# Optimization experiments

Measured on AMD Instinct MI355X. Metric: run time of the kernel, lower is better.

## Reference

```python
import jax, jax.numpy as jnp
import numpy as np

D_MODEL = 1024
NHEAD = 16
HEAD_DIM = D_MODEL // NHEAD


def setup_inputs() -> dict:
    key = jax.random.key(0)
    ks = jax.random.split(key, 7)
    B, S = 4, 2048
    scale = 1.0 / np.sqrt(D_MODEL)
    x = jax.random.normal(ks[0], (B, S, D_MODEL), dtype=jnp.float32)
    Wq = jax.random.normal(ks[1], (D_MODEL, D_MODEL), dtype=jnp.float32) * scale
    Wk = jax.random.normal(ks[2], (D_MODEL, D_MODEL), dtype=jnp.float32) * scale
    Wv = jax.random.normal(ks[3], (D_MODEL, D_MODEL), dtype=jnp.float32) * scale
    bq = jax.random.normal(ks[4], (D_MODEL,), dtype=jnp.float32) * 0.01
    bk = jax.random.normal(ks[5], (D_MODEL,), dtype=jnp.float32) * 0.01
    bv = jax.random.normal(ks[6], (D_MODEL,), dtype=jnp.float32) * 0.01
    return {"x": x, "Wq": Wq, "bq": bq, "Wk": Wk, "bk": bk, "Wv": Wv, "bv": bv}


def reference(x, Wq, bq, Wk, bk, Wv, bv):
    B, S, _ = x.shape
    # Linear projections (torch Linear: x @ W.T + b; weights here are already [in, out])
    q = x @ Wq + bq
    k = x @ Wk + bk
    v = x @ Wv + bv
    # [B, S, H, Dh] -> [B, H, S, Dh]
    q = q.reshape(B, S, NHEAD, HEAD_DIM).transpose(0, 2, 1, 3)
    k = k.reshape(B, S, NHEAD, HEAD_DIM).transpose(0, 2, 1, 3)
    v = v.reshape(B, S, NHEAD, HEAD_DIM).transpose(0, 2, 1, 3)
    # NOTE: original scales by sqrt(d_model), not sqrt(head_dim)
    scores = jnp.einsum("bhqd,bhkd->bhqk", q, k) / np.sqrt(D_MODEL).astype(np.float32)
    attn = jax.nn.softmax(scores, axis=-1)  # dropout is identity at eval
    out = jnp.einsum("bhqk,bhkd->bhqd", attn, v)
    out = out.transpose(0, 2, 1, 3).reshape(B, S, D_MODEL)
    return out
```

## Files before the change

kernel.cpp:

```cpp
#include <hip/hip_runtime.h>
#include <cstdint>
#include <cstddef>

#define SEQ 2048
#define BATCH 4
#define KVB 64
#define NT (SEQ / KVB)

typedef __attribute__((ext_vector_type(8))) unsigned short u16x8;
typedef __attribute__((ext_vector_type(8))) __bf16 bf16x8;
typedef __attribute__((ext_vector_type(4))) float f32x4;
typedef __attribute__((ext_vector_type(4))) unsigned short u16x4;

#if defined(__has_builtin)
#if __has_builtin(__builtin_amdgcn_exp2f)
#define EXP2(x) __builtin_amdgcn_exp2f(x)
#else
#define EXP2(x) exp2f(x)
#endif
#else
#define EXP2(x) exp2f(x)
#endif

static __device__ __forceinline__ unsigned short f2bf(float f) {
  unsigned u = __builtin_bit_cast(unsigned, f);
  u += 0x7fffu + ((u >> 16) & 1u);
  return (unsigned short)(u >> 16);
}

static __device__ __forceinline__ f32x4 mfma16(u16x8 a, u16x8 b, f32x4 c) {
  return __builtin_amdgcn_mfma_f32_16x16x32_bf16(
      __builtin_bit_cast(bf16x8, a), __builtin_bit_cast(bf16x8, b), c, 0, 0, 0);
}

static __device__ __forceinline__ f32x4 mfma16b(u16x8 a, bf16x8 b, f32x4 c) {
  return __builtin_amdgcn_mfma_f32_16x16x32_bf16(
      __builtin_bit_cast(bf16x8, a), b, c, 0, 0, 0);
}

static __device__ __forceinline__ void gl_lds16(const void* g, void* l) {
  __builtin_amdgcn_global_load_lds(
      (const __attribute__((address_space(1))) void*)g,
      (__attribute__((address_space(3))) void*)l, 16, 0, 0);
}

__global__ __launch_bounds__(256) void k_conv_x(const float* __restrict__ x,
                                                unsigned short* __restrict__ xb) {
  int i = (blockIdx.x * 256 + threadIdx.x) * 8;
  f32x4 a = *reinterpret_cast<const f32x4*>(x + i);
  f32x4 b = *reinterpret_cast<const f32x4*>(x + i + 4);
  u16x8 v;
  v[0] = f2bf(a[0]); v[1] = f2bf(a[1]); v[2] = f2bf(a[2]); v[3] = f2bf(a[3]);
  v[4] = f2bf(b[0]); v[5] = f2bf(b[1]); v[6] = f2bf(b[2]); v[7] = f2bf(b[3]);
  *reinterpret_cast<u16x8*>(xb + i) = v;
}

__global__ __launch_bounds__(256) void k_conv_w(const float* __restrict__ Wq,
                                                const float* __restrict__ Wk,
                                                const float* __restrict__ Wv,
                                                unsigned short* __restrict__ wt) {
  const float* W = (blockIdx.z == 0) ? Wq : (blockIdx.z == 1) ? Wk : Wv;
  unsigned short* dst = wt + (size_t)blockIdx.z * 1024 * 1024;
  __shared__ float tile[32][33];
  int n0 = blockIdx.x * 32, k0 = blockIdx.y * 32;
  int tx = threadIdx.x, ty = threadIdx.y;
#pragma unroll
  for (int i = 0; i < 4; i++) {
    int k = ty + i * 8;
    tile[k][tx] = W[(size_t)(k0 + k) * 1024 + n0 + tx];
  }
  __syncthreads();
#pragma unroll
  for (int i = 0; i < 4; i++) {
    int n = ty + i * 8;
    dst[(size_t)(n0 + n) * 1024 + k0 + tx] = f2bf(tile[tx][n]);
  }
}

__global__ __launch_bounds__(256) void k_qkv_gemm(
    const unsigned short* __restrict__ xb, const unsigned short* __restrict__ wt,
    const float* __restrict__ bq, const float* __restrict__ bk,
    const float* __restrict__ bv,
    unsigned short* __restrict__ qb, unsigned short* __restrict__ kb,
    unsigned short* __restrict__ vt) {
  __shared__ unsigned short Ah[128 * 32];
  __shared__ unsigned short Bh[128 * 32];
  const int tid = threadIdx.x;
  const int lane = tid & 63, wid = tid >> 6;
  const int ln = lane & 15, g = lane >> 4;
  const int wr = wid >> 1, wc = wid & 1;
  const int z = blockIdx.z;
  const int m0 = blockIdx.y * 128, n0 = blockIdx.x * 128;
  const unsigned short* Bt = wt + (size_t)z * 1024 * 1024;

  f32x4 acc[4][4];
#pragma unroll
  for (int i = 0; i < 4; i++)
#pragma unroll
    for (int j = 0; j < 4; j++) acc[i][j] = f32x4{0.f, 0.f, 0.f, 0.f};

  const int sA = wid * 64 + lane;
  const int rA0 = sA >> 2, cA0 = sA & 3;
  const int rA1 = rA0 + 64;

  const unsigned short* gA0 = xb + (size_t)(m0 + rA0) * 1024 + cA0 * 8;
  const unsigned short* gA1 = xb + (size_t)(m0 + rA1) * 1024 + cA0 * 8;
  const unsigned short* gB0 = Bt + (size_t)(n0 + rA0) * 1024 + cA0 * 8;
  const unsigned short* gB1 = Bt + (size_t)(n0 + rA1) * 1024 + cA0 * 8;
  unsigned short* lA0 = Ah + wid * 512;
  unsigned short* lA1 = Ah + 2048 + wid * 512;
  unsigned short* lB0 = Bh + wid * 512;
  unsigned short* lB1 = Bh + 2048 + wid * 512;

  for (int k0 = 0; k0 < 1024; k0 += 32) {
    gl_lds16(gA0 + k0, lA0);
    gl_lds16(gA1 + k0, lA1);
    gl_lds16(gB0 + k0, lB0);
    gl_lds16(gB1 + k0, lB1);
    __syncthreads();
    u16x8 af[4], bfv[4];
#pragma unroll
    for (int mi = 0; mi < 4; mi++)
      af[mi] = *reinterpret_cast<const u16x8*>(&Ah[(wr * 64 + mi * 16 + ln) * 32 + g * 8]);
#pragma unroll
    for (int ni = 0; ni < 4; ni++)
      bfv[ni] = *reinterpret_cast<const u16x8*>(&Bh[(wc * 64 + ni * 16 + ln) * 32 + g * 8]);
#pragma unroll
    for (int mi = 0; mi < 4; mi++)
#pragma unroll
      for (int ni = 0; ni < 4; ni++)
        acc[mi][ni] = mfma16(af[mi], bfv[ni], acc[mi][ni]);
    __syncthreads();
  }

  const float* bias = (z == 0) ? bq : (z == 1) ? bk : bv;
#pragma unroll
  for (int ni = 0; ni < 4; ni++) {
    int n = n0 + wc * 64 + ni * 16 + ln;
    float bb = bias[n];
    int h = n >> 6, d = n & 63;
#pragma unroll
    for (int mi = 0; mi < 4; mi++) {
      int mb = m0 + wr * 64 + mi * 16 + 4 * g;
      int b = mb >> 11, s = mb & 2047;
      if (z == 2) {
        u16x4 pv;
#pragma unroll
        for (int i = 0; i < 4; i++) pv[i] = f2bf(acc[mi][ni][i] + bb);
        int s4 = s >> 2;
        int u = s4 & 7, blk = s4 >> 3;
        int nu = ((u & 3) << 1) | (u >> 2);
        int sp = ((blk << 3) | nu) << 2;
        *reinterpret_cast<u16x4*>(
            &vt[((size_t)((b * 16 + h) * 64 + d)) * 2048 + sp]) = pv;
      } else {
        unsigned short* dst = (z == 0) ? qb : kb;
        float sc = (z == 0) ? 0.0450842200f : 1.0f;
#pragma unroll
        for (int i = 0; i < 4; i++) {
          dst[((size_t)((b * 16 + h) * 2048) + (s + i)) * 64 + d] =
              f2bf((acc[mi][ni][i] + bb) * sc);
        }
      }
    }
  }
}

__global__ __launch_bounds__(512) void k_attn(
    const unsigned short* __restrict__ qb, const unsigned short* __restrict__ kb,
    const unsigned short* __restrict__ vt, float* __restrict__ out) {
  __shared__ unsigned short Kl[2][KVB * 64];
  __shared__ unsigned short Vl[2][64 * KVB];
  const int tid = threadIdx.x;
  const int lane = tid & 63, wid = tid >> 6;
  const int ln = lane & 15, g = lane >> 4;
  const int flat = blockIdx.x;
  const int bh = flat & 63, qidx = flat >> 6;
  const int b = bh >> 4, h = bh & 15;
  const int q0 = qidx * 256 + wid * 32;
  const unsigned short* Qp = qb + (size_t)bh * SEQ * 64;
  const unsigned short* Kp = kb + (size_t)bh * SEQ * 64;
  const unsigned short* Vp = vt + (size_t)bh * 64 * SEQ;

  const int kr0 = tid >> 3;
  const int psw = ((tid & 7) ^ (kr0 & 7)) << 3;
  const unsigned short* srcK0 = Kp + (size_t)kr0 * 64 + psw;
  const unsigned short* srcV0 = Vp + (size_t)kr0 * SEQ + psw;

#define STAGE(bb, tt)                                                     \
  do {                                                                    \
    gl_lds16(srcK0 + (size_t)(tt) * (KVB * 64), &Kl[bb][wid * 512]);      \
    gl_lds16(srcV0 + (size_t)(tt) * KVB, &Vl[bb][wid * 512]);             \
  } while (0)

  u16x8 qf[2][2];
#pragma unroll
  for (int qt = 0; qt < 2; qt++)
#pragma unroll
    for (int dc = 0; dc < 2; dc++)
      qf[qt][dc] = *reinterpret_cast<const u16x8*>(
          &Qp[(size_t)(q0 + qt * 16 + ln) * 64 + dc * 32 + g * 8]);

  f32x4 o[4][2];
#pragma unroll
  for (int dt = 0; dt < 4; dt++)
#pragma unroll
    for (int qt = 0; qt < 2; qt++) o[dt][qt] = f32x4{0.f, 0.f, 0.f, 0.f};
  f32x4 lsum[2] = {f32x4{0.f, 0.f, 0.f, 0.f}, f32x4{0.f, 0.f, 0.f, 0.f}};

  u16x8 ones;
#pragma unroll
  for (int i = 0; i < 8; i++) ones[i] = 0x3F80;

  const int lm = ln & 7;
  const int ksw0 = (g ^ lm) << 3;
  const int ksw1 = ((4 + g) ^ lm) << 3;
  const int vsw0 = (g ^ lm) << 3;
  const int vsw1 = ((4 + g) ^ lm) << 3;

  int buf = 0;
  STAGE(0, 0);
  __syncthreads();

  for (int t = 0; t < NT; t++) {
    if (t + 1 < NT) STAGE(buf ^ 1, t + 1);

    const unsigned short* Kb = Kl[buf];
    const unsigned short* Vb = Vl[buf];

    u16x8 kf[4][2];
#pragma unroll
    for (int kt = 0; kt < 4; kt++) {
      int rb = (kt * 16 + ln) * 64;
      kf[kt][0] = *reinterpret_cast<const u16x8*>(&Kb[rb + ksw0]);
      kf[kt][1] = *reinterpret_cast<const u16x8*>(&Kb[rb + ksw1]);
    }

    f32x4 st[2][4];
    __builtin_amdgcn_s_setprio(1);
#pragma unroll
    for (int qt = 0; qt < 2; qt++)
#pragma unroll
      for (int kt = 0; kt < 4; kt++) {
        f32x4 c = f32x4{0.f, 0.f, 0.f, 0.f};
        c = mfma16(kf[kt][0], qf[qt][0], c);
        c = mfma16(kf[kt][1], qf[qt][1], c);
        st[qt][kt] = c;
      }
    __builtin_amdgcn_s_setprio(0);

#pragma unroll
    for (int qt = 0; qt < 2; qt++)
#pragma unroll
      for (int kt = 0; kt < 4; kt++)
#pragma unroll
        for (int i = 0; i < 4; i++)
          st[qt][kt][i] = EXP2(st[qt][kt][i]);

    bf16x8 pb[2][2];
#pragma unroll
    for (int qt = 0; qt < 2; qt++)
#pragma unroll
      for (int ks = 0; ks < 2; ks++)
#pragma unroll
        for (int i = 0; i < 4; i++) {
          pb[qt][ks][i] = (__bf16)st[qt][2 * ks][i];
          pb[qt][ks][4 + i] = (__bf16)st[qt][2 * ks + 1][i];
        }

    __builtin_amdgcn_s_setprio(1);
#pragma unroll
    for (int dt = 0; dt < 4; dt++) {
      int rb = (dt * 16 + ln) * 64;
      u16x8 vf0 = *reinterpret_cast<const u16x8*>(&Vb[rb + vsw0]);
      o[dt][0] = mfma16b(vf0, pb[0][0], o[dt][0]);
      o[dt][1] = mfma16b(vf0, pb[1][0], o[dt][1]);
      u16x8 vf1 = *reinterpret_cast<const u16x8*>(&Vb[rb + vsw1]);
      o[dt][0] = mfma16b(vf1, pb[0][1], o[dt][0]);
      o[dt][1] = mfma16b(vf1, pb[1][1], o[dt][1]);
    }
#pragma unroll
    for (int ks = 0; ks < 2; ks++) {
      lsum[0] = mfma16b(ones, pb[0][ks], lsum[0]);
      lsum[1] = mfma16b(ones, pb[1][ks], lsum[1]);
    }
    __builtin_amdgcn_s_setprio(0);

    __syncthreads();
    buf ^= 1;
  }

  float inv[2] = {1.f / lsum[0][0], 1.f / lsum[1][0]};

#pragma unroll
  for (int qt = 0; qt < 2; qt++) {
    int q = q0 + qt * 16 + ln;
#pragma unroll
    for (int dt = 0; dt < 4; dt++) {
      f32x4 r;
#pragma unroll
      for (int i = 0; i < 4; i++) r[i] = o[dt][qt][i] * inv[qt];
      *reinterpret_cast<f32x4*>(
          &out[((size_t)(b * SEQ + q)) * 1024 + h * 64 + dt * 16 + 4 * g]) = r;
    }
  }
#undef STAGE
}

extern "C" void kernel_launch(void* const* d_in, const int* in_sizes, int n_in,
                              void* d_out, int out_size, void* d_ws, size_t ws_size,
                              hipStream_t stream) {
  (void)in_sizes; (void)n_in; (void)out_size;
  const float* x  = (const float*)d_in[0];
  const float* Wq = (const float*)d_in[1];
  const float* bq = (const float*)d_in[2];
  const float* Wk = (const float*)d_in[3];
  const float* bk = (const float*)d_in[4];
  const float* Wv = (const float*)d_in[5];
  const float* bv = (const float*)d_in[6];
  float* out = (float*)d_out;

  char* ws = (char*)d_ws;
  if (ws_size < 73400320u) return;
  unsigned short* xb    = (unsigned short*)(ws);
  unsigned short* wt    = (unsigned short*)(ws + 16777216);
  unsigned short* qbuf  = (unsigned short*)(ws + 23068672);
  unsigned short* kbuf  = (unsigned short*)(ws + 39845888);
  unsigned short* vtbuf = (unsigned short*)(ws + 56623104);

  k_conv_x<<<4096, 256, 0, stream>>>(x, xb);
  k_conv_w<<<dim3(32, 32, 3), dim3(32, 8), 0, stream>>>(Wq, Wk, Wv, wt);
  k_qkv_gemm<<<dim3(8, 64, 3), 256, 0, stream>>>(xb, wt, bq, bk, bv,
                                                 qbuf, kbuf, vtbuf);
  k_attn<<<dim3(512), dim3(512), 0, stream>>>(qbuf, kbuf, vtbuf, out);
}
```

Before: 165.8 us.

## Double-buffer QKV GEMM LDS, swizzle tiles, and remap blocks per XCD

```diff
diff --git a/kernel.cpp b/kernel.cpp
--- a/kernel.cpp
+++ b/kernel.cpp
@@ -83,54 +83,66 @@
     const float* __restrict__ bv,
     unsigned short* __restrict__ qb, unsigned short* __restrict__ kb,
     unsigned short* __restrict__ vt) {
-  __shared__ unsigned short Ah[128 * 32];
-  __shared__ unsigned short Bh[128 * 32];
+  __shared__ unsigned short Ah[2][128 * 32];
+  __shared__ unsigned short Bh[2][128 * 32];
   const int tid = threadIdx.x;
   const int lane = tid & 63, wid = tid >> 6;
   const int ln = lane & 15, g = lane >> 4;
   const int wr = wid >> 1, wc = wid & 1;
-  const int z = blockIdx.z;
-  const int m0 = blockIdx.y * 128, n0 = blockIdx.x * 128;
+  const int dd = blockIdx.x;
+  const int xcd = dd & 7, j = dd >> 3;
+  const int z = j >> 6, kk = j & 63;
+  const int m0 = (((kk >> 3) << 3) | xcd) * 128;
+  const int n0 = (kk & 7) * 128;
   const unsigned short* Bt = wt + (size_t)z * 1024 * 1024;
 
   f32x4 acc[4][4];
 #pragma unroll
   for (int i = 0; i < 4; i++)
 #pragma unroll
-    for (int j = 0; j < 4; j++) acc[i][j] = f32x4{0.f, 0.f, 0.f, 0.f};
-
-  const int sA = wid * 64 + lane;
-  const int rA0 = sA >> 2, cA0 = sA & 3;
+    for (int jj = 0; jj < 4; jj++) acc[i][jj] = f32x4{0.f, 0.f, 0.f, 0.f};
+
+  const int rA0 = tid >> 2, cA0 = tid & 3;
+  const int swA = (cA0 ^ (rA0 & 3)) << 3;
   const int rA1 = rA0 + 64;
 
-  const unsigned short* gA0 = xb + (size_t)(m0 + rA0) * 1024 + cA0 * 8;
-  const unsigned short* gA1 = xb + (size_t)(m0 + rA1) * 1024 + cA0 * 8;
-  const unsigned short* gB0 = Bt + (size_t)(n0 + rA0) * 1024 + cA0 * 8;
-  const unsigned short* gB1 = Bt + (size_t)(n0 + rA1) * 1024 + cA0 * 8;
-  unsigned short* lA0 = Ah + wid * 512;
-  unsigned short* lA1 = Ah + 2048 + wid * 512;
-  unsigned short* lB0 = Bh + wid * 512;
-  unsigned short* lB1 = Bh + 2048 + wid * 512;
+  const unsigned short* gA0 = xb + (size_t)(m0 + rA0) * 1024 + swA;
+  const unsigned short* gA1 = xb + (size_t)(m0 + rA1) * 1024 + swA;
+  const unsigned short* gB0 = Bt + (size_t)(n0 + rA0) * 1024 + swA;
+  const unsigned short* gB1 = Bt + (size_t)(n0 + rA1) * 1024 + swA;
+
+#define GSTAGE(bb, k0)                                          \
+  do {                                                          \
+    gl_lds16(gA0 + (k0), &Ah[bb][wid * 512]);                   \
+    gl_lds16(gA1 + (k0), &Ah[bb][2048 + wid * 512]);            \
+    gl_lds16(gB0 + (k0), &Bh[bb][wid * 512]);                   \
+    gl_lds16(gB1 + (k0), &Bh[bb][2048 + wid * 512]);            \
+  } while (0)
+
+  const int fsw = (g ^ (ln & 3)) << 3;
+
+  int buf = 0;
+  GSTAGE(0, 0);
+  __syncthreads();
 
   for (int k0 = 0; k0 < 1024; k0 += 32) {
-    gl_lds16(gA0 + k0, lA0);
-    gl_lds16(gA1 + k0, lA1);
-    gl_lds16(gB0 + k0, lB0);
-    gl_lds16(gB1 + k0, lB1);
-    __syncthreads();
+    if (k0 + 32 < 1024) GSTAGE(buf ^ 1, k0 + 32);
     u16x8 af[4], bfv[4];
 #pragma unroll
     for (int mi = 0; mi < 4; mi++)
-      af[mi] = *reinterpret_cast<const u16x8*>(&Ah[(wr * 64 + mi * 16 + ln) * 32 + g * 8]);
+      af[mi] = *reinterpret_cast<const u16x8*>(
+          &Ah[buf][(wr * 64 + mi * 16 + ln) * 32 + fsw]);
 #pragma unroll
     for (int ni = 0; ni < 4; ni++)
-      bfv[ni] = *reinterpret_cast<const u16x8*>(&Bh[(wc * 64 + ni * 16 + ln) * 32 + g * 8]);
+      bfv[ni] = *reinterpret_cast<const u16x8*>(
+          &Bh[buf][(wc * 64 + ni * 16 + ln) * 32 + fsw]);
 #pragma unroll
     for (int mi = 0; mi < 4; mi++)
 #pragma unroll
       for (int ni = 0; ni < 4; ni++)
         acc[mi][ni] = mfma16(af[mi], bfv[ni], acc[mi][ni]);
     __syncthreads();
+    buf ^= 1;
   }
 
   const float* bias = (z == 0) ? bq : (z == 1) ? bk : bv;
@@ -164,6 +176,7 @@
       }
     }
   }
+#undef GSTAGE
 }
 
 __global__ __launch_bounds__(512) void k_attn(
@@ -330,7 +343,7 @@
 
   k_conv_x<<<4096, 256, 0, stream>>>(x, xb);
   k_conv_w<<<dim3(32, 32, 3), dim3(32, 8), 0, stream>>>(Wq, Wk, Wv, wt);
-  k_qkv_gemm<<<dim3(8, 64, 3), 256, 0, stream>>>(xb, wt, bq, bk, bv,
-                                                 qbuf, kbuf, vtbuf);
+  k_qkv_gemm<<<dim3(1536), 256, 0, stream>>>(xb, wt, bq, bk, bv,
+                                             qbuf, kbuf, vtbuf);
   k_attn<<<dim3(512), dim3(512), 0, stream>>>(qbuf, kbuf, vtbuf, out);
 }
```

New measurement: 153.4 us. 7.5% less time.
